# Kernel optimization log

Hardware: AMD Instinct MI355X
Metric: run time of the kernel (lower is better)

Reference implementation:

```python
import jax, jax.numpy as jnp
import numpy as np

B, S, D, H = 2, 2048, 1024, 16
D_H = D // H  # 64


def setup_inputs() -> dict:
    key = jax.random.key(0)
    ks = jax.random.split(key, 12)
    inp = {
        "query": jax.random.normal(ks[0], (B, S, D), dtype=jnp.float32),
        "key":   jax.random.normal(ks[1], (B, S, D), dtype=jnp.float32),
        "value": jax.random.normal(ks[2], (B, S, D), dtype=jnp.float32),
        # causal 0/1 float mask, broadcastable to [B, H, Sq, Sk]; 1 = masked
        "mask":  jnp.broadcast_to(jnp.triu(jnp.ones((S, S), dtype=jnp.float32), k=1)[None, None], (B, 1, S, S)),
    }
    scale = 0.02
    inp["wq"] = jax.random.normal(ks[3], (D, D), dtype=jnp.float32) * scale
    inp["bq"] = jnp.zeros((D,), dtype=jnp.float32)
    inp["wk"] = jax.random.normal(ks[4], (D, D), dtype=jnp.float32) * scale
    inp["bk"] = jnp.zeros((D,), dtype=jnp.float32)
    inp["wv"] = jax.random.normal(ks[5], (D, D), dtype=jnp.float32) * scale
    inp["bv"] = jnp.zeros((D,), dtype=jnp.float32)
    inp["wff"] = jax.random.normal(ks[6], (D, D), dtype=jnp.float32) * scale
    inp["bff"] = jnp.zeros((D,), dtype=jnp.float32)
    return inp


def _split_head(x):
    # [B, S, D] -> [B, H, S, d_h]
    b, s, _ = x.shape
    return x.reshape(b, s, H, D_H).transpose(0, 2, 1, 3)


def reference(query, key, value, mask, wq, bq, wk, bk, wv, bv, wff, bff):
    # QKV projections (torch Linear: x @ W.T + b)
    q = _split_head(query @ wq.T + bq)
    k = _split_head(key @ wk.T + bk)
    v = _split_head(value @ wv.T + bv)
    # scaled dot-product attention
    scores = jnp.einsum("bhqd,bhkd->bhqk", q, k) / jnp.sqrt(jnp.float32(D_H))
    scores = scores + mask * (-1e9)
    attn = jax.nn.softmax(scores, axis=-1)
    out = jnp.einsum("bhqk,bhkd->bhqd", attn, v)
    # concat heads: [B, H, S, d_h] -> [B, S, D]
    out = out.transpose(0, 2, 1, 3).reshape(query.shape[0], query.shape[1], D)
    return out @ wff.T + bff
```

## Files before the change

### kernel.cpp

```cpp
#include <hip/hip_runtime.h>
#include <hip/hip_bf16.h>

#define B_  2
#define S_  2048
#define D_  1024
#define H_  16
#define DH_ 64
#define M_  (B_ * S_)

using bf16x8 = __attribute__((ext_vector_type(8))) short;
using s16x4  = __attribute__((ext_vector_type(4))) short;
using f32x4  = __attribute__((ext_vector_type(4))) float;

__device__ __forceinline__ bf16x8 ldg8(const __hip_bfloat16* p) {
    bf16x8 v;
    __builtin_memcpy(&v, p, 16);
    return v;
}
__device__ __forceinline__ bf16x8 lds8(const __hip_bfloat16* p) {
    bf16x8 v;
    __builtin_memcpy(&v, p, 16);
    return v;
}
__device__ __forceinline__ void gll16(const void* g, void* l) {
    __builtin_amdgcn_global_load_lds(
        (const __attribute__((address_space(1))) unsigned int*)g,
        (__attribute__((address_space(3))) unsigned int*)l,
        16, 0, 0);
}

__global__ void cvt_all(const float* __restrict__ q, const float* __restrict__ k,
                        const float* __restrict__ v, const float* __restrict__ wq,
                        const float* __restrict__ wk, const float* __restrict__ wv,
                        const float* __restrict__ wff,
                        __hip_bfloat16* __restrict__ Xq, __hip_bfloat16* __restrict__ Xk,
                        __hip_bfloat16* __restrict__ Xv, __hip_bfloat16* __restrict__ Wq,
                        __hip_bfloat16* __restrict__ Wk, __hip_bfloat16* __restrict__ Wv,
                        __hip_bfloat16* __restrict__ Wf) {
    const size_t e = (size_t)(blockIdx.x * 256 + threadIdx.x) * 8;
    const float* src;
    __hip_bfloat16* dst;
    size_t off;
    if (e < ((size_t)3 << 22)) {
        const int i = (int)(e >> 22);
        off = e & (((size_t)1 << 22) - 1);
        src = (i == 0) ? q : (i == 1) ? k : v;
        dst = (i == 0) ? Xq : (i == 1) ? Xk : Xv;
    } else {
        const size_t e2 = e - ((size_t)3 << 22);
        const int i = (int)(e2 >> 20);
        off = e2 & (((size_t)1 << 20) - 1);
        src = (i == 0) ? wq : (i == 1) ? wk : (i == 2) ? wv : wff;
        dst = (i == 0) ? Wq : (i == 1) ? Wk : (i == 2) ? Wv : Wf;
    }
    float4 a, b;
    __builtin_memcpy(&a, src + off, 16);
    __builtin_memcpy(&b, src + off + 4, 16);
    __hip_bfloat16 h[8];
    h[0] = __float2bfloat16(a.x); h[1] = __float2bfloat16(a.y);
    h[2] = __float2bfloat16(a.z); h[3] = __float2bfloat16(a.w);
    h[4] = __float2bfloat16(b.x); h[5] = __float2bfloat16(b.y);
    h[6] = __float2bfloat16(b.z); h[7] = __float2bfloat16(b.w);
    __builtin_memcpy(dst + off, h, 8 * sizeof(__hip_bfloat16));
}

template<int MI>
__device__ __forceinline__
void gemm_body(const __hip_bfloat16* __restrict__ A,
               const __hip_bfloat16* __restrict__ W,
               const float* __restrict__ bias,
               void* __restrict__ out, int mode) {
    constexpr int K  = D_;
    constexpr int N  = D_;
    constexpr int TM = MI * 32;
    __shared__ __hip_bfloat16 At[2][TM][32];
    __shared__ __hip_bfloat16 Wt[2][128][32];

    const int tid = threadIdx.x;
    const int w   = tid >> 6;
    const int l   = tid & 63;
    const int lr  = l & 15;
    const int lg  = l >> 4;
    const int wr  = (w >> 1) * (MI * 16);
    const int wc  = (w & 1) * 64;
    const int row0 = blockIdx.y * TM;
    const int col0 = blockIdx.x * 128;

    const int srow   = l >> 2;
    const int schunk = l & 3;

    f32x4 acc[MI][4] = {};

    auto STAGE = [&](int buf, int k0) {
#pragma unroll
        for (int r = 0; r < TM / 64; ++r) {
            const int row = r * 64 + w * 16 + srow;
            const int csw = (schunk ^ (row & 3)) * 8;
            gll16(A + (size_t)(row0 + row) * K + k0 + csw, &At[buf][r * 64 + w * 16][0]);
        }
#pragma unroll
        for (int r = 0; r < 2; ++r) {
            const int row = r * 64 + w * 16 + srow;
            const int csw = (schunk ^ (row & 3)) * 8;
            gll16(W + (size_t)(col0 + row) * K + k0 + csw, &Wt[buf][r * 64 + w * 16][0]);
        }
    };

    STAGE(0, 0);
    int cur = 0;
    for (int k0 = 0; k0 < K; k0 += 32) {
        __syncthreads();
        if (k0 + 32 < K) STAGE(cur ^ 1, k0 + 32);
        bf16x8 af[MI], wf[4];
#pragma unroll
        for (int m = 0; m < MI; ++m) {
            const int arow = wr + m * 16 + lr;
            af[m] = lds8(&At[cur][arow][(lg ^ (arow & 3)) * 8]);
        }
#pragma unroll
        for (int n = 0; n < 4; ++n) {
            const int wrow = wc + n * 16 + lr;
            wf[n] = lds8(&Wt[cur][wrow][(lg ^ (wrow & 3)) * 8]);
        }
#pragma unroll
        for (int m = 0; m < MI; ++m)
#pragma unroll
            for (int n = 0; n < 4; ++n)
                acc[m][n] = __builtin_amdgcn_mfma_f32_16x16x32_bf16(
                    af[m], wf[n], acc[m][n], 0, 0, 0);
        cur ^= 1;
    }

    float bv[4];
#pragma unroll
    for (int n = 0; n < 4; ++n) bv[n] = bias[col0 + wc + n * 16 + lr];

    if (mode == 1) {
#pragma unroll
        for (int m = 0; m < MI; ++m) {
            const int row_s = row0 + wr + m * 16 + lg * 4;
            const int bq = row_s >> 11, s0 = row_s & (S_ - 1);
#pragma unroll
            for (int n = 0; n < 4; ++n) {
                const int col = col0 + wc + n * 16 + lr;
                const int h = col >> 6, d = col & (DH_ - 1);
                s16x4 pk;
#pragma unroll
                for (int r = 0; r < 4; ++r) {
                    __hip_bfloat16 hv = __float2bfloat16(acc[m][n][r] + bv[n]);
                    short sv;
                    __builtin_memcpy(&sv, &hv, 2);
                    pk[r] = sv;
                }
                __builtin_memcpy(
                    (__hip_bfloat16*)out + ((size_t)((bq * H_ + h) * DH_) + d) * S_ + s0,
                    &pk, 8);
            }
        }
    } else {
#pragma unroll
        for (int m = 0; m < MI; ++m)
#pragma unroll
            for (int n = 0; n < 4; ++n)
#pragma unroll
                for (int r = 0; r < 4; ++r) {
                    const int row = row0 + wr + m * 16 + lg * 4 + r;
                    const int col = col0 + wc + n * 16 + lr;
                    const float v = acc[m][n][r] + bv[n];
                    if (mode == 0)
                        ((__hip_bfloat16*)out)[(size_t)row * N + col] = __float2bfloat16(v);
                    else
                        ((float*)out)[(size_t)row * N + col] = v;
                }
    }
}

__global__ __launch_bounds__(256)
void gemm_qkv(const __hip_bfloat16* __restrict__ Xq, const __hip_bfloat16* __restrict__ Xk,
              const __hip_bfloat16* __restrict__ Xv, const __hip_bfloat16* __restrict__ Wq,
              const __hip_bfloat16* __restrict__ Wk, const __hip_bfloat16* __restrict__ Wv,
              const float* __restrict__ bq, const float* __restrict__ bk,
              const float* __restrict__ bv,
              __hip_bfloat16* __restrict__ Qp, __hip_bfloat16* __restrict__ Kp,
              __hip_bfloat16* __restrict__ Vt) {
    const int z = blockIdx.z;
    const __hip_bfloat16* A = (z == 0) ? Xq : (z == 1) ? Xk : Xv;
    const __hip_bfloat16* W = (z == 0) ? Wq : (z == 1) ? Wk : Wv;
    const float* bias       = (z == 0) ? bq : (z == 1) ? bk : bv;
    void* out               = (z == 0) ? (void*)Qp : (z == 1) ? (void*)Kp : (void*)Vt;
    gemm_body<4>(A, W, bias, out, (z == 2) ? 1 : 0);
}

__global__ __launch_bounds__(256)
void gemm_ff(const __hip_bfloat16* __restrict__ A, const __hip_bfloat16* __restrict__ W,
             const float* __restrict__ bias, float* __restrict__ out) {
    gemm_body<2>(A, W, bias, out, 2);
}

__global__ __launch_bounds__(256)
void attn_fwd(const __hip_bfloat16* __restrict__ Qp,
              const __hip_bfloat16* __restrict__ Kp,
              const __hip_bfloat16* __restrict__ Vt,
              __hip_bfloat16* __restrict__ O) {
    __shared__ __hip_bfloat16 Kt[2][64][64];
    __shared__ __hip_bfloat16 Vs[2][64][64];
    __shared__ __hip_bfloat16 Pl[4][16][64];

    const int tid = threadIdx.x;
    const int w   = tid >> 6;
    const int l   = tid & 63;
    const int lr  = l & 15;
    const int lg  = l >> 4;

    const int raw = blockIdx.x;
    const int wg  = (raw & 7) * 128 + (raw >> 3);
    const int xcd = wg >> 7;
    const int g   = (wg >> 5) & 3;
    const int c   = wg & 31;
    const int bh  = xcd * 4 + g;
    const int h   = bh & (H_ - 1);
    const int b   = bh >> 4;
    const int cc  = (g & 2) ? ((c + 16) & 31) : c;
    const int qb  = (g & 1) ? (31 - cc) : cc;
    const int q0  = qb * 64;
    const int qw0 = q0 + w * 16;

    bf16x8 aq[2];
#pragma unroll
    for (int kc = 0; kc < 2; ++kc)
        aq[kc] = ldg8(Qp + (size_t)(b * S_ + qw0 + lr) * D_ + h * DH_ + kc * 32 + lg * 8);

    f32x4 o[4] = {};
    float rs = 0.f;

    const int nkt = qb + 1;
    const float SCL = 0.125f * 1.4426950408889634f;

    const int srow   = l >> 3;
    const int schunk = l & 7;
    const int psw    = (lr & 7) << 4;

    auto STAGE = [&](int buf, int kt) {
        const int k0 = kt * 64;
#pragma unroll
        for (int r = 0; r < 2; ++r) {
            const int row = r * 32 + w * 8 + srow;
            const int csw = (schunk ^ (row & 7)) * 8;
            gll16(Kp + (size_t)(b * S_ + k0 + row) * D_ + h * DH_ + csw,
                  &Kt[buf][r * 32 + w * 8][0]);
            gll16(Vt + ((size_t)((b * H_ + h) * DH_) + row) * S_ + k0 + csw,
                  &Vs[buf][r * 32 + w * 8][0]);
        }
    };

    char* prow = (char*)&Pl[w][lr][0];

    STAGE(0, 0);
    int cur = 0;
    for (int kt = 0; kt < nkt; ++kt) {
        const int k0 = kt * 64;
        __syncthreads();
        if (kt + 1 < nkt) STAGE(cur ^ 1, kt + 1);

        f32x4 sc[4] = {};
#pragma unroll
        for (int kk = 0; kk < 4; ++kk) {
            const int krow = kk * 16 + lr;
#pragma unroll
            for (int kc = 0; kc < 2; ++kc) {
                bf16x8 kf = lds8(&Kt[cur][krow][((kc * 4 + lg) ^ (krow & 7)) * 8]);
                sc[kk] = __builtin_amdgcn_mfma_f32_16x16x32_bf16(kf, aq[kc], sc[kk], 0, 0, 0);
            }
        }

        const int qrow = qw0 + lr;
        if (kt == qb) {
#pragma unroll
            for (int kk = 0; kk < 4; ++kk) {
                s16x4 pk;
#pragma unroll
                for (int r = 0; r < 4; ++r) {
                    const int key = k0 + kk * 16 + lg * 4 + r;
                    const float p = (key > qrow) ? 0.f : exp2f(sc[kk][r] * SCL);
                    rs += p;
                    __hip_bfloat16 hv = __float2bfloat16(p);
                    short sv; __builtin_memcpy(&sv, &hv, 2);
                    pk[r] = sv;
                }
                __builtin_memcpy(prow + ((kk * 32 + lg * 8) ^ psw), &pk, 8);
            }
        } else {
#pragma unroll
            for (int kk = 0; kk < 4; ++kk) {
                s16x4 pk;
#pragma unroll
                for (int r = 0; r < 4; ++r) {
                    const float p = exp2f(sc[kk][r] * SCL);
                    rs += p;
                    __hip_bfloat16 hv = __float2bfloat16(p);
                    short sv; __builtin_memcpy(&sv, &hv, 2);
                    pk[r] = sv;
                }
                __builtin_memcpy(prow + ((kk * 32 + lg * 8) ^ psw), &pk, 8);
            }
        }

        bf16x8 pa[2];
#pragma unroll
        for (int kc = 0; kc < 2; ++kc)
            __builtin_memcpy(&pa[kc], prow + ((kc * 64 + lg * 16) ^ psw), 16);
#pragma unroll
        for (int j = 0; j < 4; ++j) {
            const int vrow = j * 16 + lr;
#pragma unroll
            for (int kc = 0; kc < 2; ++kc) {
                bf16x8 vf = lds8(&Vs[cur][vrow][((kc * 4 + lg) ^ (vrow & 7)) * 8]);
                o[j] = __builtin_amdgcn_mfma_f32_16x16x32_bf16(pa[kc], vf, o[j], 0, 0, 0);
            }
        }
        cur ^= 1;
    }

    float rsf = rs;
    rsf += __shfl_xor(rsf, 16);
    rsf += __shfl_xor(rsf, 32);
#pragma unroll
    for (int r = 0; r < 4; ++r) {
        const float inv = 1.f / __shfl(rsf, 4 * lg + r);
        const int row = qw0 + 4 * lg + r;
#pragma unroll
        for (int j = 0; j < 4; ++j)
            O[((size_t)(b * S_ + row)) * D_ + h * DH_ + j * 16 + lr] =
                __float2bfloat16(o[j][r] * inv);
    }
}

extern "C" void kernel_launch(void* const* d_in, const int* in_sizes, int n_in,
                              void* d_out, int out_size, void* d_ws, size_t ws_size,
                              hipStream_t stream) {
    const float* q    = (const float*)d_in[0];
    const float* kin  = (const float*)d_in[1];
    const float* vin  = (const float*)d_in[2];
    const float* wq   = (const float*)d_in[4];
    const float* bq   = (const float*)d_in[5];
    const float* wk   = (const float*)d_in[6];
    const float* bk   = (const float*)d_in[7];
    const float* wv   = (const float*)d_in[8];
    const float* bv   = (const float*)d_in[9];
    const float* wff  = (const float*)d_in[10];
    const float* bff  = (const float*)d_in[11];

    char* ws = (char*)d_ws;
    const size_t MB = 1024 * 1024;
    __hip_bfloat16* Xq  = (__hip_bfloat16*)(ws + 0 * MB);
    __hip_bfloat16* Xk  = (__hip_bfloat16*)(ws + 8 * MB);
    __hip_bfloat16* Xv  = (__hip_bfloat16*)(ws + 16 * MB);
    __hip_bfloat16* Wqb = (__hip_bfloat16*)(ws + 24 * MB);
    __hip_bfloat16* Wkb = (__hip_bfloat16*)(ws + 26 * MB);
    __hip_bfloat16* Wvb = (__hip_bfloat16*)(ws + 28 * MB);
    __hip_bfloat16* Wfb = (__hip_bfloat16*)(ws + 30 * MB);
    __hip_bfloat16* Qp  = (__hip_bfloat16*)(ws + 32 * MB);
    __hip_bfloat16* Kp  = (__hip_bfloat16*)(ws + 40 * MB);
    __hip_bfloat16* Vt  = (__hip_bfloat16*)(ws + 48 * MB);
    __hip_bfloat16* Ob  = (__hip_bfloat16*)(ws + 56 * MB);

    cvt_all<<<8192, 256, 0, stream>>>(q, kin, vin, wq, wk, wv, wff,
                                      Xq, Xk, Xv, Wqb, Wkb, Wvb, Wfb);

    dim3 gq(D_ / 128, M_ / 128, 3);
    gemm_qkv<<<gq, 256, 0, stream>>>(Xq, Xk, Xv, Wqb, Wkb, Wvb,
                                     bq, bk, bv, Qp, Kp, Vt);

    attn_fwd<<<B_ * H_ * (S_ / 64), 256, 0, stream>>>(Qp, Kp, Vt, Ob);

    dim3 gg(D_ / 128, M_ / 64);
    gemm_ff<<<gg, 256, 0, stream>>>(Ob, Wfb, bff, (float*)d_out);
}
```

Measured before the change: 133.0 us.

## Fuse fp32-to-bf16 activation conversion into QKV GEMM and pair causal query blocks

The QKV GEMM now loads fp32 activations into registers, converts them to bf16 and writes them to LDS, so the separate activation conversion pass and its extra global round trip are removed. Only the weights are still converted up front. The attention kernel now uses 512-thread blocks, each pairing a short and a long causal query block so every block does the same total work, and it raises wave priority around the MFMA sections. The risks are register-staged A loads that hide latency less well than direct-to-LDS loads, and idle waves at barriers when one half of a block finishes before the other.

```diff
diff --git a/kernel.cpp b/kernel.cpp
--- a/kernel.cpp
+++ b/kernel.cpp
@@ -28,31 +28,22 @@
         (__attribute__((address_space(3))) unsigned int*)l,
         16, 0, 0);
 }
-
-__global__ void cvt_all(const float* __restrict__ q, const float* __restrict__ k,
-                        const float* __restrict__ v, const float* __restrict__ wq,
-                        const float* __restrict__ wk, const float* __restrict__ wv,
-                        const float* __restrict__ wff,
-                        __hip_bfloat16* __restrict__ Xq, __hip_bfloat16* __restrict__ Xk,
-                        __hip_bfloat16* __restrict__ Xv, __hip_bfloat16* __restrict__ Wq,
-                        __hip_bfloat16* __restrict__ Wk, __hip_bfloat16* __restrict__ Wv,
-                        __hip_bfloat16* __restrict__ Wf) {
+__device__ __forceinline__ short bf16bits(float x) {
+    __hip_bfloat16 hv = __float2bfloat16(x);
+    short sv;
+    __builtin_memcpy(&sv, &hv, 2);
+    return sv;
+}
+
+__global__ void cvt_w(const float* __restrict__ wq, const float* __restrict__ wk,
+                      const float* __restrict__ wv, const float* __restrict__ wff,
+                      __hip_bfloat16* __restrict__ Wq, __hip_bfloat16* __restrict__ Wk,
+                      __hip_bfloat16* __restrict__ Wv, __hip_bfloat16* __restrict__ Wf) {
     const size_t e = (size_t)(blockIdx.x * 256 + threadIdx.x) * 8;
-    const float* src;
-    __hip_bfloat16* dst;
-    size_t off;
-    if (e < ((size_t)3 << 22)) {
-        const int i = (int)(e >> 22);
-        off = e & (((size_t)1 << 22) - 1);
-        src = (i == 0) ? q : (i == 1) ? k : v;
-        dst = (i == 0) ? Xq : (i == 1) ? Xk : Xv;
-    } else {
-        const size_t e2 = e - ((size_t)3 << 22);
-        const int i = (int)(e2 >> 20);
-        off = e2 & (((size_t)1 << 20) - 1);
-        src = (i == 0) ? wq : (i == 1) ? wk : (i == 2) ? wv : wff;
-        dst = (i == 0) ? Wq : (i == 1) ? Wk : (i == 2) ? Wv : Wf;
-    }
+    const int i = (int)(e >> 20);
+    const size_t off = e & (((size_t)1 << 20) - 1);
+    const float* src = (i == 0) ? wq : (i == 1) ? wk : (i == 2) ? wv : wff;
+    __hip_bfloat16* dst = (i == 0) ? Wq : (i == 1) ? Wk : (i == 2) ? Wv : Wf;
     float4 a, b;
     __builtin_memcpy(&a, src + off, 16);
     __builtin_memcpy(&b, src + off + 4, 16);
@@ -61,12 +52,12 @@
     h[2] = __float2bfloat16(a.z); h[3] = __float2bfloat16(a.w);
     h[4] = __float2bfloat16(b.x); h[5] = __float2bfloat16(b.y);
     h[6] = __float2bfloat16(b.z); h[7] = __float2bfloat16(b.w);
-    __builtin_memcpy(dst + off, h, 8 * sizeof(__hip_bfloat16));
-}
-
-template<int MI>
+    __builtin_memcpy(dst + off, h, 16);
+}
+
+template<int MI, bool AF32>
 __device__ __forceinline__
-void gemm_body(const __hip_bfloat16* __restrict__ A,
+void gemm_body(const void* __restrict__ Ap,
                const __hip_bfloat16* __restrict__ W,
                const float* __restrict__ bias,
                void* __restrict__ out, int mode) {
@@ -86,31 +77,65 @@
     const int row0 = blockIdx.y * TM;
     const int col0 = blockIdx.x * 128;
 
-    const int srow   = l >> 2;
-    const int schunk = l & 3;
+    const int wsrow   = l >> 2;
+    const int wschunk = l & 3;
+
+    const int arow_r = tid >> 3;
+    const int acol   = (tid & 7) * 4;
+    const int achunk = (tid & 7) >> 1;
+    const int ahalf  = tid & 1;
 
     f32x4 acc[MI][4] = {};
-
-    auto STAGE = [&](int buf, int k0) {
+    f32x4 ar[TM / 32];
+
+    auto LOADA = [&](int k0) {
+#pragma unroll
+        for (int r = 0; r < TM / 32; ++r) {
+            const int row = r * 32 + arow_r;
+            __builtin_memcpy(&ar[r],
+                             (const float*)Ap + (size_t)(row0 + row) * K + k0 + acol, 16);
+        }
+    };
+    auto WRITEA = [&](int buf) {
+#pragma unroll
+        for (int r = 0; r < TM / 32; ++r) {
+            const int row = r * 32 + arow_r;
+            s16x4 pk;
+#pragma unroll
+            for (int j = 0; j < 4; ++j) pk[j] = bf16bits(ar[r][j]);
+            char* dst = (char*)&At[buf][row][0] + ((achunk ^ (row & 3)) * 16 + ahalf * 8);
+            __builtin_memcpy(dst, &pk, 8);
+        }
+    };
+    auto STAGEA_BF = [&](int buf, int k0) {
 #pragma unroll
         for (int r = 0; r < TM / 64; ++r) {
-            const int row = r * 64 + w * 16 + srow;
-            const int csw = (schunk ^ (row & 3)) * 8;
-            gll16(A + (size_t)(row0 + row) * K + k0 + csw, &At[buf][r * 64 + w * 16][0]);
-        }
+            const int row = r * 64 + w * 16 + wsrow;
+            const int csw = (wschunk ^ (row & 3)) * 8;
+            gll16((const __hip_bfloat16*)Ap + (size_t)(row0 + row) * K + k0 + csw,
+                  &At[buf][r * 64 + w * 16][0]);
+        }
+    };
+    auto STAGEW = [&](int buf, int k0) {
 #pragma unroll
         for (int r = 0; r < 2; ++r) {
-            const int row = r * 64 + w * 16 + srow;
-            const int csw = (schunk ^ (row & 3)) * 8;
+            const int row = r * 64 + w * 16 + wsrow;
+            const int csw = (wschunk ^ (row & 3)) * 8;
             gll16(W + (size_t)(col0 + row) * K + k0 + csw, &Wt[buf][r * 64 + w * 16][0]);
         }
     };
 
-    STAGE(0, 0);
+    if (AF32) { LOADA(0); WRITEA(0); } else STAGEA_BF(0, 0);
+    STAGEW(0, 0);
     int cur = 0;
     for (int k0 = 0; k0 < K; k0 += 32) {
         __syncthreads();
-        if (k0 + 32 < K) STAGE(cur ^ 1, k0 + 32);
+        const bool more = (k0 + 32 < K);
+        if (more) {
+            STAGEW(cur ^ 1, k0 + 32);
+            if (AF32) LOADA(k0 + 32);
+            else      STAGEA_BF(cur ^ 1, k0 + 32);
+        }
         bf16x8 af[MI], wf[4];
 #pragma unroll
         for (int m = 0; m < MI; ++m) {
@@ -128,6 +153,7 @@
             for (int n = 0; n < 4; ++n)
                 acc[m][n] = __builtin_amdgcn_mfma_f32_16x16x32_bf16(
                     af[m], wf[n], acc[m][n], 0, 0, 0);
+        if (AF32 && more) WRITEA(cur ^ 1);
         cur ^= 1;
     }
 
@@ -146,12 +172,7 @@
                 const int h = col >> 6, d = col & (DH_ - 1);
                 s16x4 pk;
 #pragma unroll
-                for (int r = 0; r < 4; ++r) {
-                    __hip_bfloat16 hv = __float2bfloat16(acc[m][n][r] + bv[n]);
-                    short sv;
-                    __builtin_memcpy(&sv, &hv, 2);
-                    pk[r] = sv;
-                }
+                for (int r = 0; r < 4; ++r) pk[r] = bf16bits(acc[m][n][r] + bv[n]);
                 __builtin_memcpy(
                     (__hip_bfloat16*)out + ((size_t)((bq * H_ + h) * DH_) + d) * S_ + s0,
                     &pk, 8);
@@ -176,35 +197,35 @@
 }
 
 __global__ __launch_bounds__(256)
-void gemm_qkv(const __hip_bfloat16* __restrict__ Xq, const __hip_bfloat16* __restrict__ Xk,
-              const __hip_bfloat16* __restrict__ Xv, const __hip_bfloat16* __restrict__ Wq,
+void gemm_qkv(const float* __restrict__ Xq, const float* __restrict__ Xk,
+              const float* __restrict__ Xv, const __hip_bfloat16* __restrict__ Wq,
               const __hip_bfloat16* __restrict__ Wk, const __hip_bfloat16* __restrict__ Wv,
               const float* __restrict__ bq, const float* __restrict__ bk,
               const float* __restrict__ bv,
               __hip_bfloat16* __restrict__ Qp, __hip_bfloat16* __restrict__ Kp,
               __hip_bfloat16* __restrict__ Vt) {
     const int z = blockIdx.z;
-    const __hip_bfloat16* A = (z == 0) ? Xq : (z == 1) ? Xk : Xv;
+    const void* A           = (z == 0) ? (const void*)Xq : (z == 1) ? (const void*)Xk : (const void*)Xv;
     const __hip_bfloat16* W = (z == 0) ? Wq : (z == 1) ? Wk : Wv;
     const float* bias       = (z == 0) ? bq : (z == 1) ? bk : bv;
     void* out               = (z == 0) ? (void*)Qp : (z == 1) ? (void*)Kp : (void*)Vt;
-    gemm_body<4>(A, W, bias, out, (z == 2) ? 1 : 0);
+    gemm_body<4, true>(A, W, bias, out, (z == 2) ? 1 : 0);
 }
 
 __global__ __launch_bounds__(256)
 void gemm_ff(const __hip_bfloat16* __restrict__ A, const __hip_bfloat16* __restrict__ W,
              const float* __restrict__ bias, float* __restrict__ out) {
-    gemm_body<2>(A, W, bias, out, 2);
-}
-
-__global__ __launch_bounds__(256)
+    gemm_body<2, false>(A, W, bias, out, 2);
+}
+
+__global__ __launch_bounds__(512)
 void attn_fwd(const __hip_bfloat16* __restrict__ Qp,
               const __hip_bfloat16* __restrict__ Kp,
               const __hip_bfloat16* __restrict__ Vt,
               __hip_bfloat16* __restrict__ O) {
     __shared__ __hip_bfloat16 Kt[2][64][64];
     __shared__ __hip_bfloat16 Vs[2][64][64];
-    __shared__ __hip_bfloat16 Pl[4][16][64];
+    __shared__ __hip_bfloat16 Pl[8][16][64];
 
     const int tid = threadIdx.x;
     const int w   = tid >> 6;
@@ -213,17 +234,19 @@
     const int lg  = l >> 4;
 
     const int raw = blockIdx.x;
-    const int wg  = (raw & 7) * 128 + (raw >> 3);
-    const int xcd = wg >> 7;
-    const int g   = (wg >> 5) & 3;
-    const int c   = wg & 31;
-    const int bh  = xcd * 4 + g;
+    const int wg  = (raw & 7) * 64 + (raw >> 3);
+    const int xcd = wg >> 6;
+    const int loc = wg & 63;
+    const int bhi = loc >> 4;
+    const int prr = loc & 15;
+    const int pr  = (bhi >= 2) ? (15 - prr) : prr;
+    const int bh  = xcd * 4 + bhi;
     const int h   = bh & (H_ - 1);
     const int b   = bh >> 4;
-    const int cc  = (g & 2) ? ((c + 16) & 31) : c;
-    const int qb  = (g & 1) ? (31 - cc) : cc;
-    const int q0  = qb * 64;
-    const int qw0 = q0 + w * 16;
+
+    const int sub  = w >> 2;
+    const int qb_s = sub ? (31 - pr) : pr;
+    const int qw0  = qb_s * 64 + (w & 3) * 16;
 
     bf16x8 aq[2];
 #pragma unroll
@@ -233,7 +256,7 @@
     f32x4 o[4] = {};
     float rs = 0.f;
 
-    const int nkt = qb + 1;
+    const int nkt_max = 32 - pr;
     const float SCL = 0.125f * 1.4426950408889634f;
 
     const int srow   = l >> 3;
@@ -242,81 +265,80 @@
 
     auto STAGE = [&](int buf, int kt) {
         const int k0 = kt * 64;
-#pragma unroll
-        for (int r = 0; r < 2; ++r) {
-            const int row = r * 32 + w * 8 + srow;
-            const int csw = (schunk ^ (row & 7)) * 8;
-            gll16(Kp + (size_t)(b * S_ + k0 + row) * D_ + h * DH_ + csw,
-                  &Kt[buf][r * 32 + w * 8][0]);
-            gll16(Vt + ((size_t)((b * H_ + h) * DH_) + row) * S_ + k0 + csw,
-                  &Vs[buf][r * 32 + w * 8][0]);
-        }
+        const int row = w * 8 + srow;
+        const int csw = (schunk ^ (row & 7)) * 8;
+        gll16(Kp + (size_t)(b * S_ + k0 + row) * D_ + h * DH_ + csw,
+              &Kt[buf][w * 8][0]);
+        gll16(Vt + ((size_t)((b * H_ + h) * DH_) + row) * S_ + k0 + csw,
+              &Vs[buf][w * 8][0]);
     };
 
     char* prow = (char*)&Pl[w][lr][0];
 
     STAGE(0, 0);
     int cur = 0;
-    for (int kt = 0; kt < nkt; ++kt) {
+    for (int kt = 0; kt < nkt_max; ++kt) {
         const int k0 = kt * 64;
         __syncthreads();
-        if (kt + 1 < nkt) STAGE(cur ^ 1, kt + 1);
-
-        f32x4 sc[4] = {};
-#pragma unroll
-        for (int kk = 0; kk < 4; ++kk) {
-            const int krow = kk * 16 + lr;
-#pragma unroll
-            for (int kc = 0; kc < 2; ++kc) {
-                bf16x8 kf = lds8(&Kt[cur][krow][((kc * 4 + lg) ^ (krow & 7)) * 8]);
-                sc[kk] = __builtin_amdgcn_mfma_f32_16x16x32_bf16(kf, aq[kc], sc[kk], 0, 0, 0);
+        if (kt + 1 < nkt_max) STAGE(cur ^ 1, kt + 1);
+
+        if (kt <= qb_s) {
+            f32x4 sc[4] = {};
+            __builtin_amdgcn_s_setprio(1);
+#pragma unroll
+            for (int kk = 0; kk < 4; ++kk) {
+                const int krow = kk * 16 + lr;
+#pragma unroll
+                for (int kc = 0; kc < 2; ++kc) {
+                    bf16x8 kf = lds8(&Kt[cur][krow][((kc * 4 + lg) ^ (krow & 7)) * 8]);
+                    sc[kk] = __builtin_amdgcn_mfma_f32_16x16x32_bf16(kf, aq[kc], sc[kk], 0, 0, 0);
+                }
             }
-        }
-
-        const int qrow = qw0 + lr;
-        if (kt == qb) {
-#pragma unroll
-            for (int kk = 0; kk < 4; ++kk) {
-                s16x4 pk;
-#pragma unroll
-                for (int r = 0; r < 4; ++r) {
-                    const int key = k0 + kk * 16 + lg * 4 + r;
-                    const float p = (key > qrow) ? 0.f : exp2f(sc[kk][r] * SCL);
-                    rs += p;
-                    __hip_bfloat16 hv = __float2bfloat16(p);
-                    short sv; __builtin_memcpy(&sv, &hv, 2);
-                    pk[r] = sv;
-                }
-                __builtin_memcpy(prow + ((kk * 32 + lg * 8) ^ psw), &pk, 8);
+            __builtin_amdgcn_s_setprio(0);
+
+            const int qrow = qw0 + lr;
+            if (kt == qb_s) {
+#pragma unroll
+                for (int kk = 0; kk < 4; ++kk) {
+                    s16x4 pk;
+#pragma unroll
+                    for (int r = 0; r < 4; ++r) {
+                        const int key = k0 + kk * 16 + lg * 4 + r;
+                        const float p = (key > qrow) ? 0.f : exp2f(sc[kk][r] * SCL);
+                        rs += p;
+                        pk[r] = bf16bits(p);
+                    }
+                    __builtin_memcpy(prow + ((kk * 32 + lg * 8) ^ psw), &pk, 8);
+                }
+            } else {
+#pragma unroll
+                for (int kk = 0; kk < 4; ++kk) {
+                    s16x4 pk;
+#pragma unroll
+                    for (int r = 0; r < 4; ++r) {
+                        const float p = exp2f(sc[kk][r] * SCL);
+                        rs += p;
+                        pk[r] = bf16bits(p);
+                    }
+                    __builtin_memcpy(prow + ((kk * 32 + lg * 8) ^ psw), &pk, 8);
+                }
             }
-        } else {
-#pragma unroll
-            for (int kk = 0; kk < 4; ++kk) {
-                s16x4 pk;
-#pragma unroll
-                for (int r = 0; r < 4; ++r) {
-                    const float p = exp2f(sc[kk][r] * SCL);
-                    rs += p;
-                    __hip_bfloat16 hv = __float2bfloat16(p);
-                    short sv; __builtin_memcpy(&sv, &hv, 2);
-                    pk[r] = sv;
-                }
-                __builtin_memcpy(prow + ((kk * 32 + lg * 8) ^ psw), &pk, 8);
+
+            bf16x8 pa[2];
+#pragma unroll
+            for (int kc = 0; kc < 2; ++kc)
+                __builtin_memcpy(&pa[kc], prow + ((kc * 64 + lg * 16) ^ psw), 16);
+            __builtin_amdgcn_s_setprio(1);
+#pragma unroll
+            for (int j = 0; j < 4; ++j) {
+                const int vrow = j * 16 + lr;
+#pragma unroll
+                for (int kc = 0; kc < 2; ++kc) {
+                    bf16x8 vf = lds8(&Vs[cur][vrow][((kc * 4 + lg) ^ (vrow & 7)) * 8]);
+                    o[j] = __builtin_amdgcn_mfma_f32_16x16x32_bf16(pa[kc], vf, o[j], 0, 0, 0);
+                }
             }
-        }
-
-        bf16x8 pa[2];
-#pragma unroll
-        for (int kc = 0; kc < 2; ++kc)
-            __builtin_memcpy(&pa[kc], prow + ((kc * 64 + lg * 16) ^ psw), 16);
-#pragma unroll
-        for (int j = 0; j < 4; ++j) {
-            const int vrow = j * 16 + lr;
-#pragma unroll
-            for (int kc = 0; kc < 2; ++kc) {
-                bf16x8 vf = lds8(&Vs[cur][vrow][((kc * 4 + lg) ^ (vrow & 7)) * 8]);
-                o[j] = __builtin_amdgcn_mfma_f32_16x16x32_bf16(pa[kc], vf, o[j], 0, 0, 0);
-            }
+            __builtin_amdgcn_s_setprio(0);
         }
         cur ^= 1;
     }
@@ -352,9 +374,6 @@
 
     char* ws = (char*)d_ws;
     const size_t MB = 1024 * 1024;
-    __hip_bfloat16* Xq  = (__hip_bfloat16*)(ws + 0 * MB);
-    __hip_bfloat16* Xk  = (__hip_bfloat16*)(ws + 8 * MB);
-    __hip_bfloat16* Xv  = (__hip_bfloat16*)(ws + 16 * MB);
     __hip_bfloat16* Wqb = (__hip_bfloat16*)(ws + 24 * MB);
     __hip_bfloat16* Wkb = (__hip_bfloat16*)(ws + 26 * MB);
     __hip_bfloat16* Wvb = (__hip_bfloat16*)(ws + 28 * MB);
@@ -364,14 +383,13 @@
     __hip_bfloat16* Vt  = (__hip_bfloat16*)(ws + 48 * MB);
     __hip_bfloat16* Ob  = (__hip_bfloat16*)(ws + 56 * MB);
 
-    cvt_all<<<8192, 256, 0, stream>>>(q, kin, vin, wq, wk, wv, wff,
-                                      Xq, Xk, Xv, Wqb, Wkb, Wvb, Wfb);
+    cvt_w<<<2048, 256, 0, stream>>>(wq, wk, wv, wff, Wqb, Wkb, Wvb, Wfb);
 
     dim3 gq(D_ / 128, M_ / 128, 3);
-    gemm_qkv<<<gq, 256, 0, stream>>>(Xq, Xk, Xv, Wqb, Wkb, Wvb,
+    gemm_qkv<<<gq, 256, 0, stream>>>(q, kin, vin, Wqb, Wkb, Wvb,
                                      bq, bk, bv, Qp, Kp, Vt);
 
-    attn_fwd<<<B_ * H_ * (S_ / 64), 256, 0, stream>>>(Qp, Kp, Vt, Ob);
+    attn_fwd<<<512, 512, 0, stream>>>(Qp, Kp, Vt, Ob);
 
     dim3 gg(D_ / 128, M_ / 64);
     gemm_ff<<<gg, 256, 0, stream>>>(Ob, Wfb, bff, (float*)d_out);
```

New measurement: 154.1 us. 1.16x slower.

## Pair causal q-blocks per 512-thread attention block to share K/V staging

Applied to the files above, without the earlier changes.

The attention kernel now launches 512 blocks of 512 threads, and each block handles two complementary query tiles (pr and 31-pr) of the same head. The two tiles share the K/V tiles staged in LDS, and the block loops to the longer tile's length while the shorter tile's waves sit idle once past their diagonal. This balances causal work across blocks and halves the number of K/V loads. It also adds s_setprio around the MFMA sections to favour matrix issue. Costs are higher LDS and thread count per block and idle waves in the shorter half.

```diff
diff --git a/kernel.cpp b/kernel.cpp
--- a/kernel.cpp
+++ b/kernel.cpp
@@ -27,6 +27,12 @@
         (const __attribute__((address_space(1))) unsigned int*)g,
         (__attribute__((address_space(3))) unsigned int*)l,
         16, 0, 0);
+}
+__device__ __forceinline__ short bf16bits(float x) {
+    __hip_bfloat16 hv = __float2bfloat16(x);
+    short sv;
+    __builtin_memcpy(&sv, &hv, 2);
+    return sv;
 }
 
 __global__ void cvt_all(const float* __restrict__ q, const float* __restrict__ k,
@@ -61,7 +67,7 @@
     h[2] = __float2bfloat16(a.z); h[3] = __float2bfloat16(a.w);
     h[4] = __float2bfloat16(b.x); h[5] = __float2bfloat16(b.y);
     h[6] = __float2bfloat16(b.z); h[7] = __float2bfloat16(b.w);
-    __builtin_memcpy(dst + off, h, 8 * sizeof(__hip_bfloat16));
+    __builtin_memcpy(dst + off, h, 16);
 }
 
 template<int MI>
@@ -146,12 +152,7 @@
                 const int h = col >> 6, d = col & (DH_ - 1);
                 s16x4 pk;
 #pragma unroll
-                for (int r = 0; r < 4; ++r) {
-                    __hip_bfloat16 hv = __float2bfloat16(acc[m][n][r] + bv[n]);
-                    short sv;
-                    __builtin_memcpy(&sv, &hv, 2);
-                    pk[r] = sv;
-                }
+                for (int r = 0; r < 4; ++r) pk[r] = bf16bits(acc[m][n][r] + bv[n]);
                 __builtin_memcpy(
                     (__hip_bfloat16*)out + ((size_t)((bq * H_ + h) * DH_) + d) * S_ + s0,
                     &pk, 8);
@@ -197,14 +198,14 @@
     gemm_body<2>(A, W, bias, out, 2);
 }
 
-__global__ __launch_bounds__(256)
+__global__ __launch_bounds__(512)
 void attn_fwd(const __hip_bfloat16* __restrict__ Qp,
               const __hip_bfloat16* __restrict__ Kp,
               const __hip_bfloat16* __restrict__ Vt,
               __hip_bfloat16* __restrict__ O) {
     __shared__ __hip_bfloat16 Kt[2][64][64];
     __shared__ __hip_bfloat16 Vs[2][64][64];
-    __shared__ __hip_bfloat16 Pl[4][16][64];
+    __shared__ __hip_bfloat16 Pl[8][16][64];
 
     const int tid = threadIdx.x;
     const int w   = tid >> 6;
@@ -213,17 +214,19 @@
     const int lg  = l >> 4;
 
     const int raw = blockIdx.x;
-    const int wg  = (raw & 7) * 128 + (raw >> 3);
-    const int xcd = wg >> 7;
-    const int g   = (wg >> 5) & 3;
-    const int c   = wg & 31;
-    const int bh  = xcd * 4 + g;
+    const int wg  = (raw & 7) * 64 + (raw >> 3);
+    const int xcd = wg >> 6;
+    const int loc = wg & 63;
+    const int bhi = loc >> 4;
+    const int prr = loc & 15;
+    const int pr  = (bhi >= 2) ? (15 - prr) : prr;
+    const int bh  = xcd * 4 + bhi;
     const int h   = bh & (H_ - 1);
     const int b   = bh >> 4;
-    const int cc  = (g & 2) ? ((c + 16) & 31) : c;
-    const int qb  = (g & 1) ? (31 - cc) : cc;
-    const int q0  = qb * 64;
-    const int qw0 = q0 + w * 16;
+
+    const int sub  = w >> 2;
+    const int qb_s = sub ? (31 - pr) : pr;
+    const int qw0  = qb_s * 64 + (w & 3) * 16;
 
     bf16x8 aq[2];
 #pragma unroll
@@ -233,7 +236,7 @@
     f32x4 o[4] = {};
     float rs = 0.f;
 
-    const int nkt = qb + 1;
+    const int nkt_max = 32 - pr;
     const float SCL = 0.125f * 1.4426950408889634f;
 
     const int srow   = l >> 3;
@@ -242,81 +245,80 @@
 
     auto STAGE = [&](int buf, int kt) {
         const int k0 = kt * 64;
-#pragma unroll
-        for (int r = 0; r < 2; ++r) {
-            const int row = r * 32 + w * 8 + srow;
-            const int csw = (schunk ^ (row & 7)) * 8;
-            gll16(Kp + (size_t)(b * S_ + k0 + row) * D_ + h * DH_ + csw,
-                  &Kt[buf][r * 32 + w * 8][0]);
-            gll16(Vt + ((size_t)((b * H_ + h) * DH_) + row) * S_ + k0 + csw,
-                  &Vs[buf][r * 32 + w * 8][0]);
-        }
+        const int row = w * 8 + srow;
+        const int csw = (schunk ^ (row & 7)) * 8;
+        gll16(Kp + (size_t)(b * S_ + k0 + row) * D_ + h * DH_ + csw,
+              &Kt[buf][w * 8][0]);
+        gll16(Vt + ((size_t)((b * H_ + h) * DH_) + row) * S_ + k0 + csw,
+              &Vs[buf][w * 8][0]);
     };
 
     char* prow = (char*)&Pl[w][lr][0];
 
     STAGE(0, 0);
     int cur = 0;
-    for (int kt = 0; kt < nkt; ++kt) {
+    for (int kt = 0; kt < nkt_max; ++kt) {
         const int k0 = kt * 64;
         __syncthreads();
-        if (kt + 1 < nkt) STAGE(cur ^ 1, kt + 1);
-
-        f32x4 sc[4] = {};
-#pragma unroll
-        for (int kk = 0; kk < 4; ++kk) {
-            const int krow = kk * 16 + lr;
-#pragma unroll
-            for (int kc = 0; kc < 2; ++kc) {
-                bf16x8 kf = lds8(&Kt[cur][krow][((kc * 4 + lg) ^ (krow & 7)) * 8]);
-                sc[kk] = __builtin_amdgcn_mfma_f32_16x16x32_bf16(kf, aq[kc], sc[kk], 0, 0, 0);
+        if (kt + 1 < nkt_max) STAGE(cur ^ 1, kt + 1);
+
+        if (kt <= qb_s) {
+            f32x4 sc[4] = {};
+            __builtin_amdgcn_s_setprio(1);
+#pragma unroll
+            for (int kk = 0; kk < 4; ++kk) {
+                const int krow = kk * 16 + lr;
+#pragma unroll
+                for (int kc = 0; kc < 2; ++kc) {
+                    bf16x8 kf = lds8(&Kt[cur][krow][((kc * 4 + lg) ^ (krow & 7)) * 8]);
+                    sc[kk] = __builtin_amdgcn_mfma_f32_16x16x32_bf16(kf, aq[kc], sc[kk], 0, 0, 0);
+                }
             }
-        }
-
-        const int qrow = qw0 + lr;
-        if (kt == qb) {
-#pragma unroll
-            for (int kk = 0; kk < 4; ++kk) {
-                s16x4 pk;
-#pragma unroll
-                for (int r = 0; r < 4; ++r) {
-                    const int key = k0 + kk * 16 + lg * 4 + r;
-                    const float p = (key > qrow) ? 0.f : exp2f(sc[kk][r] * SCL);
-                    rs += p;
-                    __hip_bfloat16 hv = __float2bfloat16(p);
-                    short sv; __builtin_memcpy(&sv, &hv, 2);
-                    pk[r] = sv;
-                }
-                __builtin_memcpy(prow + ((kk * 32 + lg * 8) ^ psw), &pk, 8);
+            __builtin_amdgcn_s_setprio(0);
+
+            const int qrow = qw0 + lr;
+            if (kt == qb_s) {
+#pragma unroll
+                for (int kk = 0; kk < 4; ++kk) {
+                    s16x4 pk;
+#pragma unroll
+                    for (int r = 0; r < 4; ++r) {
+                        const int key = k0 + kk * 16 + lg * 4 + r;
+                        const float p = (key > qrow) ? 0.f : exp2f(sc[kk][r] * SCL);
+                        rs += p;
+                        pk[r] = bf16bits(p);
+                    }
+                    __builtin_memcpy(prow + ((kk * 32 + lg * 8) ^ psw), &pk, 8);
+                }
+            } else {
+#pragma unroll
+                for (int kk = 0; kk < 4; ++kk) {
+                    s16x4 pk;
+#pragma unroll
+                    for (int r = 0; r < 4; ++r) {
+                        const float p = exp2f(sc[kk][r] * SCL);
+                        rs += p;
+                        pk[r] = bf16bits(p);
+                    }
+                    __builtin_memcpy(prow + ((kk * 32 + lg * 8) ^ psw), &pk, 8);
+                }
             }
-        } else {
-#pragma unroll
-            for (int kk = 0; kk < 4; ++kk) {
-                s16x4 pk;
-#pragma unroll
-                for (int r = 0; r < 4; ++r) {
-                    const float p = exp2f(sc[kk][r] * SCL);
-                    rs += p;
-                    __hip_bfloat16 hv = __float2bfloat16(p);
-                    short sv; __builtin_memcpy(&sv, &hv, 2);
-                    pk[r] = sv;
-                }
-                __builtin_memcpy(prow + ((kk * 32 + lg * 8) ^ psw), &pk, 8);
+
+            bf16x8 pa[2];
+#pragma unroll
+            for (int kc = 0; kc < 2; ++kc)
+                __builtin_memcpy(&pa[kc], prow + ((kc * 64 + lg * 16) ^ psw), 16);
+            __builtin_amdgcn_s_setprio(1);
+#pragma unroll
+            for (int j = 0; j < 4; ++j) {
+                const int vrow = j * 16 + lr;
+#pragma unroll
+                for (int kc = 0; kc < 2; ++kc) {
+                    bf16x8 vf = lds8(&Vs[cur][vrow][((kc * 4 + lg) ^ (vrow & 7)) * 8]);
+                    o[j] = __builtin_amdgcn_mfma_f32_16x16x32_bf16(pa[kc], vf, o[j], 0, 0, 0);
+                }
             }
-        }
-
-        bf16x8 pa[2];
-#pragma unroll
-        for (int kc = 0; kc < 2; ++kc)
-            __builtin_memcpy(&pa[kc], prow + ((kc * 64 + lg * 16) ^ psw), 16);
-#pragma unroll
-        for (int j = 0; j < 4; ++j) {
-            const int vrow = j * 16 + lr;
-#pragma unroll
-            for (int kc = 0; kc < 2; ++kc) {
-                bf16x8 vf = lds8(&Vs[cur][vrow][((kc * 4 + lg) ^ (vrow & 7)) * 8]);
-                o[j] = __builtin_amdgcn_mfma_f32_16x16x32_bf16(pa[kc], vf, o[j], 0, 0, 0);
-            }
+            __builtin_amdgcn_s_setprio(0);
         }
         cur ^= 1;
     }
@@ -371,7 +373,7 @@
     gemm_qkv<<<gq, 256, 0, stream>>>(Xq, Xk, Xv, Wqb, Wkb, Wvb,
                                      bq, bk, bv, Qp, Kp, Vt);
 
-    attn_fwd<<<B_ * H_ * (S_ / 64), 256, 0, stream>>>(Qp, Kp, Vt, Ob);
+    attn_fwd<<<512, 512, 0, stream>>>(Qp, Kp, Vt, Ob);
 
     dim3 gg(D_ / 128, M_ / 64);
     gemm_ff<<<gg, 256, 0, stream>>>(Ob, Wfb, bff, (float*)d_out);
```

Result: faster. 125.8 us (-5.4%).
